# Performance work log

Measured on AMD Instinct MI355X. Metric: run time of the kernel, lower is better.

The kernel has to match this reference:

```python
import jax, jax.numpy as jnp
import numpy as np

B, C, T, H, W = 4, 256, 16, 16, 16
C2 = C // 2  # 128


def setup_inputs() -> dict:
    key = jax.random.key(0)
    ks = jax.random.split(key, 12)
    s = 1.0 / np.sqrt(C)
    return {
        "X": jax.random.normal(ks[0], (B, C, T, H, W), dtype=jnp.float32),
        "pe": jax.random.uniform(ks[1], (C, T, H, W), dtype=jnp.float32),
        "task_q": jax.random.uniform(ks[2], (C2, T, H, W), dtype=jnp.float32),
        "task_k": jax.random.uniform(ks[3], (C2, T, H, W), dtype=jnp.float32),
        "task_v": jax.random.uniform(ks[4], (C2, T, H, W), dtype=jnp.float32),
        "Wq": jax.random.normal(ks[5], (C2, C), dtype=jnp.float32) * s,
        "bq": jnp.zeros((C2,), dtype=jnp.float32),
        "Wk": jax.random.normal(ks[6], (C2, C), dtype=jnp.float32) * s,
        "bk": jnp.zeros((C2,), dtype=jnp.float32),
        "Wv": jax.random.normal(ks[7], (C2, C), dtype=jnp.float32) * s,
        "bv": jnp.zeros((C2,), dtype=jnp.float32),
        "Wo": jax.random.normal(ks[8], (C, C2), dtype=jnp.float32) * s,
    }


def reference(X, pe, task_q, task_k, task_v, Wq, bq, Wk, bk, Wv, bv, Wo):
    b, c, t, h, w = X.shape
    c2 = Wq.shape[0]
    n = t * h * w
    Xp = X + pe  # broadcast [C,T,H,W] over batch

    def proj(Wm, bm, task):
        # 1x1x1 Conv3d == channel contraction; add bias and per-task offset
        y = jnp.einsum('bcthw,oc->bothw', Xp, Wm)
        return y + bm[:, None, None, None] + task  # [B,C2,T,H,W]

    q = proj(Wq, bq, task_q).reshape(b, c2, n).transpose(0, 2, 1)  # [B,N,C2]
    k = proj(Wk, bk, task_k).reshape(b, c2, n)                     # [B,C2,N]
    sim = jnp.matmul(q, k)                                         # [B,N,N]
    v = proj(Wv, bv, task_v).reshape(b, c2, n).transpose(0, 2, 1)  # [B,N,C2]
    # NOTE: original torch code computes softmax(sim) but then multiplies by
    # the RAW similarity matrix (softmax output is dead code). Faithful math:
    out = jnp.matmul(sim, v)                                       # [B,N,C2]
    # torch .reshape of contiguous [B,N,C2] -> [B,C2,T,H,W] (layout reinterpret)
    out = out.reshape(b, c2, t, h, w)
    out = jnp.einsum('bcthw,oc->bothw', out, Wo)  # out_conv, no bias
    return out + X
```

## Files before the change

kernel.cpp:

```cpp
#include <hip/hip_runtime.h>
#include <cstddef>

#define BB 4
#define CCH 256
#define C2 128
#define NN 4096
#define PM 384
#define KVS 16

typedef __attribute__((ext_vector_type(8))) short short8v;
typedef __attribute__((ext_vector_type(4))) short short4v;
typedef __attribute__((ext_vector_type(4))) float f32x4;

static __device__ __forceinline__ short f2bf(float f) {
    union { float f; unsigned u; } c; c.f = f;
    unsigned r = (c.u + 0x7FFFu + ((c.u >> 16) & 1u)) >> 16;
    return (short)r;
}

__global__ __launch_bounds__(256) void k_pack(
    const float* __restrict__ Wq, const float* __restrict__ bq,
    const float* __restrict__ Wk, const float* __restrict__ bk,
    const float* __restrict__ Wv, const float* __restrict__ bv,
    const float* __restrict__ Wo,
    short* __restrict__ wpackh, float* __restrict__ bpack,
    short* __restrict__ Woh)
{
    const int m = blockIdx.x;
    const int c = threadIdx.x;
    if (m < PM) {
        const float* w; const float* bs; int mm;
        if (m < C2)        { w = Wq; bs = bq; mm = m; }
        else if (m < 2*C2) { w = Wk; bs = bk; mm = m - C2; }
        else               { w = Wv; bs = bv; mm = m - 2*C2; }
        wpackh[m * CCH + c] = f2bf(w[mm * CCH + c]);
        if (c == 0) bpack[m] = bs[mm];
    } else {
        const int o = m - PM;
        if (c < C2) Woh[o * C2 + c] = f2bf(Wo[o * C2 + c]);
    }
}

#define LROW 40
#define TSP  136
__global__ __launch_bounds__(256) void k_projm(
    const float* __restrict__ X, const float* __restrict__ pe,
    const float* __restrict__ tq, const float* __restrict__ tk,
    const float* __restrict__ tv,
    const short* __restrict__ wpackh, const float* __restrict__ bpack,
    short* __restrict__ qt, short* __restrict__ kk, short* __restrict__ vv)
{
    __shared__ short smem[17408];
    short* As = smem;
    short* Bs = smem + 5120;
    const int b  = blockIdx.z;
    const int m0 = blockIdx.y * 128;
    const int n0 = blockIdx.x * 128;
    const int tid  = threadIdx.x;
    const int wave = tid >> 6;
    const int lane = tid & 63;
    const int lr = lane & 15, lg = lane >> 4;
    const int wm = wave >> 1, wn = wave & 1;
    const float* __restrict__ Xb = X + (size_t)b * CCH * NN;

    const int am  = tid >> 1;
    const int akb = tid & 1;
    const int cq  = tid >> 5;
    const int nq  = tid & 31;

    f32x4 acc[4][4];
#pragma unroll
    for (int i = 0; i < 4; ++i)
#pragma unroll
        for (int j = 0; j < 4; ++j) acc[i][j] = (f32x4){0.f, 0.f, 0.f, 0.f};

    for (int k0 = 0; k0 < CCH; k0 += 32) {
        {
            const size_t gsrc = (size_t)(m0 + am) * CCH + k0 + akb * 16;
            *(short8v*)&As[am * LROW + akb * 16]     = *(const short8v*)&wpackh[gsrc];
            *(short8v*)&As[am * LROW + akb * 16 + 8] = *(const short8v*)&wpackh[gsrc + 8];
        }
        short sreg[4][4];
#pragma unroll
        for (int j = 0; j < 4; ++j) {
            const int c = k0 + cq * 4 + j;
            const size_t g = (size_t)c * NN + n0 + nq * 4;
            float4 x4 = *(const float4*)&Xb[g];
            float4 p4 = *(const float4*)&pe[g];
            sreg[j][0] = f2bf(x4.x + p4.x);
            sreg[j][1] = f2bf(x4.y + p4.y);
            sreg[j][2] = f2bf(x4.z + p4.z);
            sreg[j][3] = f2bf(x4.w + p4.w);
        }
#pragma unroll
        for (int i = 0; i < 4; ++i) {
            short4v v; v.x = sreg[0][i]; v.y = sreg[1][i]; v.z = sreg[2][i]; v.w = sreg[3][i];
            *(short4v*)&Bs[(nq * 4 + i) * LROW + cq * 4] = v;
        }
        __syncthreads();
        short8v a[4], bfr[4];
#pragma unroll
        for (int fm = 0; fm < 4; ++fm)
            a[fm] = *(const short8v*)&As[(wm * 64 + fm * 16 + lr) * LROW + lg * 8];
#pragma unroll
        for (int fn = 0; fn < 4; ++fn)
            bfr[fn] = *(const short8v*)&Bs[(wn * 64 + fn * 16 + lr) * LROW + lg * 8];
#pragma unroll
        for (int fm = 0; fm < 4; ++fm)
#pragma unroll
            for (int fn = 0; fn < 4; ++fn)
                acc[fm][fn] = __builtin_amdgcn_mfma_f32_16x16x32_bf16(
                    a[fm], bfr[fn], acc[fm][fn], 0, 0, 0);
        __syncthreads();
    }

    short* Ts = smem;
    const int sel = m0 >> 7;
    if (sel == 0) {
#pragma unroll
        for (int fm = 0; fm < 4; ++fm)
#pragma unroll
            for (int fn = 0; fn < 4; ++fn) {
                const int n_l  = wn * 64 + fn * 16 + lr;
                const int m_lb = wm * 64 + fm * 16 + lg * 4;
                short4v v;
#pragma unroll
                for (int r = 0; r < 4; ++r) {
                    const int m_l = m_lb + r;
                    v[r] = f2bf(acc[fm][fn][r] + bpack[m_l]
                                + tq[(size_t)m_l * NN + n0 + n_l]);
                }
                *(short4v*)&Ts[n_l * TSP + m_lb] = v;
            }
        __syncthreads();
        const int n_l = tid >> 1, half = tid & 1;
        short* dst = qt + (size_t)b * NN * C2 + (size_t)(n0 + n_l) * C2 + half * 64;
        const short* src = &Ts[n_l * TSP + half * 64];
#pragma unroll
        for (int q2 = 0; q2 < 8; ++q2)
            *(short8v*)&dst[q2 * 8] = *(const short8v*)&src[q2 * 8];
    } else {
        const float* __restrict__ task = (sel == 1) ? tk : tv;
        short* kv = (sel == 1) ? kk : vv;
#pragma unroll
        for (int fm = 0; fm < 4; ++fm)
#pragma unroll
            for (int fn = 0; fn < 4; ++fn) {
                const int n_l = wn * 64 + fn * 16 + lr;
#pragma unroll
                for (int r = 0; r < 4; ++r) {
                    const int m_l = wm * 64 + fm * 16 + lg * 4 + r;
                    Ts[m_l * TSP + n_l] =
                        f2bf(acc[fm][fn][r] + bpack[m0 + m_l]
                             + task[(size_t)m_l * NN + n0 + n_l]);
                }
            }
        __syncthreads();
        const int m_l = tid >> 1, half = tid & 1;
        short* dst = kv + (size_t)b * C2 * NN + (size_t)m_l * NN + n0 + half * 64;
        const short* src = &Ts[m_l * TSP + half * 64];
#pragma unroll
        for (int q2 = 0; q2 < 8; ++q2)
            *(short8v*)&dst[q2 * 8] = *(const short8v*)&src[q2 * 8];
    }
}

__global__ __launch_bounds__(256) void k_kv(
    const short* __restrict__ kk, const short* __restrict__ vv,
    float* __restrict__ Mpart)
{
    const int b = blockIdx.y, s = blockIdx.x;
    const int tid = threadIdx.x;
    const int wave = tid >> 6, lane = tid & 63;
    const int lr = lane & 15, lg = lane >> 4;
    const int wi = wave >> 1, wj = wave & 1;
    const short* Kb = kk + (size_t)b * C2 * NN;
    const short* Vb = vv + (size_t)b * C2 * NN;
    const int nbase = s * 256;
    f32x4 acc[4][4];
#pragma unroll
    for (int i = 0; i < 4; ++i)
#pragma unroll
        for (int j = 0; j < 4; ++j) acc[i][j] = (f32x4){0.f, 0.f, 0.f, 0.f};

    for (int ks = 0; ks < 8; ++ks) {
        const int nn = nbase + ks * 32 + lg * 8;
        short8v a[4], bv8[4];
#pragma unroll
        for (int fi = 0; fi < 4; ++fi)
            a[fi] = *(const short8v*)&Kb[(size_t)(wi * 64 + fi * 16 + lr) * NN + nn];
#pragma unroll
        for (int fj = 0; fj < 4; ++fj)
            bv8[fj] = *(const short8v*)&Vb[(size_t)(wj * 64 + fj * 16 + lr) * NN + nn];
#pragma unroll
        for (int fi = 0; fi < 4; ++fi)
#pragma unroll
            for (int fj = 0; fj < 4; ++fj)
                acc[fi][fj] = __builtin_amdgcn_mfma_f32_16x16x32_bf16(
                    a[fi], bv8[fj], acc[fi][fj], 0, 0, 0);
    }
    float* Mp = Mpart + ((size_t)b * KVS + s) * C2 * C2;
#pragma unroll
    for (int fi = 0; fi < 4; ++fi)
#pragma unroll
        for (int fj = 0; fj < 4; ++fj) {
            const int j = wj * 64 + fj * 16 + lr;
#pragma unroll
            for (int r = 0; r < 4; ++r) {
                const int i = wi * 64 + fi * 16 + lg * 4 + r;
                Mp[(size_t)i * C2 + j] = acc[fi][fj][r];
            }
        }
}

__global__ __launch_bounds__(256) void k_kvred(
    const float* __restrict__ Mpart, short* __restrict__ Mt)
{
    const int b = blockIdx.y;
    const int i = blockIdx.x * 16 + (threadIdx.x >> 4);
    const int j0 = (threadIdx.x & 15) * 8;
    const float* p = Mpart + (size_t)b * KVS * C2 * C2 + (size_t)i * C2 + j0;
    float a8[8];
#pragma unroll
    for (int e = 0; e < 8; ++e) a8[e] = 0.f;
    for (int s = 0; s < KVS; ++s) {
        float4 v0 = *(const float4*)&p[(size_t)s * C2 * C2];
        float4 v1 = *(const float4*)&p[(size_t)s * C2 * C2 + 4];
        a8[0] += v0.x; a8[1] += v0.y; a8[2] += v0.z; a8[3] += v0.w;
        a8[4] += v1.x; a8[5] += v1.y; a8[6] += v1.z; a8[7] += v1.w;
    }
    short* mt = Mt + (size_t)b * C2 * C2;
#pragma unroll
    for (int e = 0; e < 8; ++e)
        mt[(size_t)(j0 + e) * C2 + i] = f2bf(a8[e]);
}

__global__ __launch_bounds__(256) void k_qm(
    const short* __restrict__ qt, const short* __restrict__ Mt,
    short* __restrict__ out3)
{
    const int b = blockIdx.y;
    const int n0 = blockIdx.x * 128;
    const int tid = threadIdx.x;
    const int wave = tid >> 6, lane = tid & 63;
    const int lr = lane & 15, lg = lane >> 4;
    const int wj = wave >> 1, wn = wave & 1;
    const short* Mb = Mt + (size_t)b * C2 * C2;
    const short* Qb = qt + (size_t)b * NN * C2;
    f32x4 acc[4][4];
#pragma unroll
    for (int i = 0; i < 4; ++i)
#pragma unroll
        for (int j = 0; j < 4; ++j) acc[i][j] = (f32x4){0.f, 0.f, 0.f, 0.f};

    for (int ks = 0; ks < 4; ++ks) {
        const int kb = ks * 32 + lg * 8;
        short8v a[4], bq8[4];
#pragma unroll
        for (int fj = 0; fj < 4; ++fj)
            a[fj] = *(const short8v*)&Mb[(size_t)(wj * 64 + fj * 16 + lr) * C2 + kb];
#pragma unroll
        for (int fn = 0; fn < 4; ++fn)
            bq8[fn] = *(const short8v*)&Qb[(size_t)(n0 + wn * 64 + fn * 16 + lr) * C2 + kb];
#pragma unroll
        for (int fj = 0; fj < 4; ++fj)
#pragma unroll
            for (int fn = 0; fn < 4; ++fn)
                acc[fj][fn] = __builtin_amdgcn_mfma_f32_16x16x32_bf16(
                    a[fj], bq8[fn], acc[fj][fn], 0, 0, 0);
    }
    short* O3 = out3 + (size_t)b * NN * C2;
#pragma unroll
    for (int fj = 0; fj < 4; ++fj)
#pragma unroll
        for (int fn = 0; fn < 4; ++fn) {
            const int n  = n0 + wn * 64 + fn * 16 + lr;
            const int jb = wj * 64 + fj * 16 + lg * 4;
            short4v v;
#pragma unroll
            for (int r = 0; r < 4; ++r) v[r] = f2bf(acc[fj][fn][r]);
            *(short4v*)&O3[(size_t)n * C2 + jb] = v;
        }
}

__global__ __launch_bounds__(256) void k_final(
    const short* __restrict__ out3, const short* __restrict__ Woh,
    const float* __restrict__ X, float* __restrict__ out)
{
    const int g  = blockIdx.x;
    const int o0 = blockIdx.y * 128;
    const int b  = blockIdx.z;
    const int tid = threadIdx.x;
    const int wave = tid >> 6, lane = tid & 63;
    const int lr = lane & 15, lg = lane >> 4;
    const int wm = wave >> 1, wn = wave & 1;
    const short* O3 = out3 + (size_t)b * NN * C2;
    f32x4 acc[4][4];
#pragma unroll
    for (int i = 0; i < 4; ++i)
#pragma unroll
        for (int j = 0; j < 4; ++j) acc[i][j] = (f32x4){0.f, 0.f, 0.f, 0.f};

    for (int ks = 0; ks < 4; ++ks) {
        const int c0 = ks * 32;
        short8v a[4], bb[4];
#pragma unroll
        for (int fm = 0; fm < 4; ++fm)
            a[fm] = *(const short8v*)&Woh[(size_t)(o0 + wm * 64 + fm * 16 + lr) * C2
                                          + c0 + lg * 8];
#pragma unroll
        for (int fn = 0; fn < 4; ++fn) {
            const int pj = wn * 64 + fn * 16 + lr;
            short8v t;
#pragma unroll
            for (int e = 0; e < 8; ++e)
                t[e] = O3[(size_t)((c0 + lg * 8 + e) * 32 + g) * C2 + pj];
            bb[fn] = t;
        }
#pragma unroll
        for (int fm = 0; fm < 4; ++fm)
#pragma unroll
            for (int fn = 0; fn < 4; ++fn)
                acc[fm][fn] = __builtin_amdgcn_mfma_f32_16x16x32_bf16(
                    a[fm], bb[fn], acc[fm][fn], 0, 0, 0);
    }
    const float* Xb = X + (size_t)b * CCH * NN;
    float* Ob = out + (size_t)b * CCH * NN;
#pragma unroll
    for (int fm = 0; fm < 4; ++fm)
#pragma unroll
        for (int fn = 0; fn < 4; ++fn) {
            const int p  = g * 128 + wn * 64 + fn * 16 + lr;
            const int ob = o0 + wm * 64 + fm * 16 + lg * 4;
#pragma unroll
            for (int r = 0; r < 4; ++r) {
                const size_t ad = (size_t)(ob + r) * NN + p;
                Ob[ad] = acc[fm][fn][r] + Xb[ad];
            }
        }
}

extern "C" void kernel_launch(void* const* d_in, const int* in_sizes, int n_in,
                              void* d_out, int out_size, void* d_ws, size_t ws_size,
                              hipStream_t stream) {
    const float* X  = (const float*)d_in[0];
    const float* pe = (const float*)d_in[1];
    const float* tq = (const float*)d_in[2];
    const float* tk = (const float*)d_in[3];
    const float* tv = (const float*)d_in[4];
    const float* Wq = (const float*)d_in[5];
    const float* bq = (const float*)d_in[6];
    const float* Wk = (const float*)d_in[7];
    const float* bk = (const float*)d_in[8];
    const float* Wv = (const float*)d_in[9];
    const float* bv = (const float*)d_in[10];
    const float* Wo = (const float*)d_in[11];
    float* out = (float*)d_out;

    float* ws     = (float*)d_ws;
    float* bpack  = ws;
    short* wpackh = (short*)(ws + 512);
    short* Woh    = (short*)(ws + 512 + 49152);
    short* qt     = (short*)(ws + 512 + 49152 + 16384);
    short* kk     = qt + (size_t)BB * NN * C2;
    short* vv     = kk + (size_t)BB * NN * C2;
    short* out3   = vv + (size_t)BB * NN * C2;
    short* Mt     = out3 + (size_t)BB * NN * C2;
    float* Mpart  = (float*)(Mt + (size_t)BB * C2 * C2);

    k_pack<<<dim3(PM + CCH), dim3(256), 0, stream>>>(
        Wq, bq, Wk, bk, Wv, bv, Wo, wpackh, bpack, Woh);
    k_projm<<<dim3(NN / 128, 3, BB), dim3(256), 0, stream>>>(
        X, pe, tq, tk, tv, wpackh, bpack, qt, kk, vv);
    k_kv<<<dim3(KVS, BB), dim3(256), 0, stream>>>(kk, vv, Mpart);
    k_kvred<<<dim3(8, BB), dim3(256), 0, stream>>>(Mpart, Mt);
    k_qm<<<dim3(NN / 128, BB), dim3(256), 0, stream>>>(qt, Mt, out3);
    k_final<<<dim3(32, 2, BB), dim3(256), 0, stream>>>(out3, Woh, X, out);
}
```

Before: 139.3 us.

## Precompute bf16 X+pe, split KV reduction finer, fuse Q·M with output projection

Adds a pre-pass that converts X+pe to bf16 once, so the projection kernel no longer re-reads and re-adds fp32 X and pe for each of its three row blocks. The K·V partial reduction is split into twice as many slices for more parallelism. The Q·M product and the output 1x1 conv are fused into one kernel that holds the intermediate tile in shared memory instead of writing and re-reading out3. The cost is an extra launch and a workspace buffer for Xp, which Mpart now shares (aliases).

New measurement: 149.1 us. 1.07x slower.

```diff
diff --git a/kernel.cpp b/kernel.cpp
--- a/kernel.cpp
+++ b/kernel.cpp
@@ -6,7 +6,7 @@
 #define C2 128
 #define NN 4096
 #define PM 384
-#define KVS 16
+#define KVS 32
 
 typedef __attribute__((ext_vector_type(8))) short short8v;
 typedef __attribute__((ext_vector_type(4))) short short4v;
@@ -41,10 +41,28 @@
     }
 }
 
+__global__ __launch_bounds__(256) void k_xph(
+    const float* __restrict__ X, const float* __restrict__ pe,
+    short* __restrict__ XpH)
+{
+    const size_t e8 = ((size_t)blockIdx.x * 256 + threadIdx.x) * 8;
+    const size_t r  = e8 & (size_t)(CCH * NN - 1);
+    float4 x0 = *(const float4*)&X[e8];
+    float4 x1 = *(const float4*)&X[e8 + 4];
+    float4 p0 = *(const float4*)&pe[r];
+    float4 p1 = *(const float4*)&pe[r + 4];
+    short8v o;
+    o[0] = f2bf(x0.x + p0.x); o[1] = f2bf(x0.y + p0.y);
+    o[2] = f2bf(x0.z + p0.z); o[3] = f2bf(x0.w + p0.w);
+    o[4] = f2bf(x1.x + p1.x); o[5] = f2bf(x1.y + p1.y);
+    o[6] = f2bf(x1.z + p1.z); o[7] = f2bf(x1.w + p1.w);
+    *(short8v*)&XpH[e8] = o;
+}
+
 #define LROW 40
 #define TSP  136
 __global__ __launch_bounds__(256) void k_projm(
-    const float* __restrict__ X, const float* __restrict__ pe,
+    const short* __restrict__ XpH,
     const float* __restrict__ tq, const float* __restrict__ tk,
     const float* __restrict__ tv,
     const short* __restrict__ wpackh, const float* __restrict__ bpack,
@@ -61,7 +79,7 @@
     const int lane = tid & 63;
     const int lr = lane & 15, lg = lane >> 4;
     const int wm = wave >> 1, wn = wave & 1;
-    const float* __restrict__ Xb = X + (size_t)b * CCH * NN;
+    const short* __restrict__ Xb = XpH + (size_t)b * CCH * NN;
 
     const int am  = tid >> 1;
     const int akb = tid & 1;
@@ -84,13 +102,8 @@
 #pragma unroll
         for (int j = 0; j < 4; ++j) {
             const int c = k0 + cq * 4 + j;
-            const size_t g = (size_t)c * NN + n0 + nq * 4;
-            float4 x4 = *(const float4*)&Xb[g];
-            float4 p4 = *(const float4*)&pe[g];
-            sreg[j][0] = f2bf(x4.x + p4.x);
-            sreg[j][1] = f2bf(x4.y + p4.y);
-            sreg[j][2] = f2bf(x4.z + p4.z);
-            sreg[j][3] = f2bf(x4.w + p4.w);
+            short4v xv = *(const short4v*)&Xb[(size_t)c * NN + n0 + nq * 4];
+            sreg[j][0] = xv.x; sreg[j][1] = xv.y; sreg[j][2] = xv.z; sreg[j][3] = xv.w;
         }
 #pragma unroll
         for (int i = 0; i < 4; ++i) {
@@ -176,14 +189,14 @@
     const int wi = wave >> 1, wj = wave & 1;
     const short* Kb = kk + (size_t)b * C2 * NN;
     const short* Vb = vv + (size_t)b * C2 * NN;
-    const int nbase = s * 256;
+    const int nbase = s * 128;
     f32x4 acc[4][4];
 #pragma unroll
     for (int i = 0; i < 4; ++i)
 #pragma unroll
         for (int j = 0; j < 4; ++j) acc[i][j] = (f32x4){0.f, 0.f, 0.f, 0.f};
 
-    for (int ks = 0; ks < 8; ++ks) {
+    for (int ks = 0; ks < 4; ++ks) {
         const int nn = nbase + ks * 32 + lg * 8;
         short8v a[4], bv8[4];
 #pragma unroll
@@ -235,109 +248,102 @@
         mt[(size_t)(j0 + e) * C2 + i] = f2bf(a8[e]);
 }
 
-__global__ __launch_bounds__(256) void k_qm(
+#define PSP 136
+__global__ __launch_bounds__(256) void k_qmfinal(
     const short* __restrict__ qt, const short* __restrict__ Mt,
-    short* __restrict__ out3)
-{
-    const int b = blockIdx.y;
-    const int n0 = blockIdx.x * 128;
-    const int tid = threadIdx.x;
-    const int wave = tid >> 6, lane = tid & 63;
-    const int lr = lane & 15, lg = lane >> 4;
-    const int wj = wave >> 1, wn = wave & 1;
-    const short* Mb = Mt + (size_t)b * C2 * C2;
-    const short* Qb = qt + (size_t)b * NN * C2;
-    f32x4 acc[4][4];
-#pragma unroll
-    for (int i = 0; i < 4; ++i)
-#pragma unroll
-        for (int j = 0; j < 4; ++j) acc[i][j] = (f32x4){0.f, 0.f, 0.f, 0.f};
-
-    for (int ks = 0; ks < 4; ++ks) {
-        const int kb = ks * 32 + lg * 8;
-        short8v a[4], bq8[4];
-#pragma unroll
-        for (int fj = 0; fj < 4; ++fj)
-            a[fj] = *(const short8v*)&Mb[(size_t)(wj * 64 + fj * 16 + lr) * C2 + kb];
-#pragma unroll
-        for (int fn = 0; fn < 4; ++fn)
-            bq8[fn] = *(const short8v*)&Qb[(size_t)(n0 + wn * 64 + fn * 16 + lr) * C2 + kb];
-#pragma unroll
-        for (int fj = 0; fj < 4; ++fj)
-#pragma unroll
-            for (int fn = 0; fn < 4; ++fn)
-                acc[fj][fn] = __builtin_amdgcn_mfma_f32_16x16x32_bf16(
-                    a[fj], bq8[fn], acc[fj][fn], 0, 0, 0);
-    }
-    short* O3 = out3 + (size_t)b * NN * C2;
-#pragma unroll
-    for (int fj = 0; fj < 4; ++fj)
-#pragma unroll
-        for (int fn = 0; fn < 4; ++fn) {
-            const int n  = n0 + wn * 64 + fn * 16 + lr;
-            const int jb = wj * 64 + fj * 16 + lg * 4;
-            short4v v;
-#pragma unroll
-            for (int r = 0; r < 4; ++r) v[r] = f2bf(acc[fj][fn][r]);
-            *(short4v*)&O3[(size_t)n * C2 + jb] = v;
-        }
-}
-
-__global__ __launch_bounds__(256) void k_final(
-    const short* __restrict__ out3, const short* __restrict__ Woh,
+    const short* __restrict__ Woh,
     const float* __restrict__ X, float* __restrict__ out)
 {
+    __shared__ short Ps[64 * PSP];
     const int g  = blockIdx.x;
-    const int o0 = blockIdx.y * 128;
+    const int jh = blockIdx.y;
     const int b  = blockIdx.z;
     const int tid = threadIdx.x;
     const int wave = tid >> 6, lane = tid & 63;
     const int lr = lane & 15, lg = lane >> 4;
-    const int wm = wave >> 1, wn = wave & 1;
-    const short* O3 = out3 + (size_t)b * NN * C2;
-    f32x4 acc[4][4];
-#pragma unroll
-    for (int i = 0; i < 4; ++i)
-#pragma unroll
-        for (int j = 0; j < 4; ++j) acc[i][j] = (f32x4){0.f, 0.f, 0.f, 0.f};
-
-    for (int ks = 0; ks < 4; ++ks) {
-        const int c0 = ks * 32;
-        short8v a[4], bb[4];
-#pragma unroll
-        for (int fm = 0; fm < 4; ++fm)
-            a[fm] = *(const short8v*)&Woh[(size_t)(o0 + wm * 64 + fm * 16 + lr) * C2
-                                          + c0 + lg * 8];
-#pragma unroll
-        for (int fn = 0; fn < 4; ++fn) {
-            const int pj = wn * 64 + fn * 16 + lr;
-            short8v t;
-#pragma unroll
-            for (int e = 0; e < 8; ++e)
-                t[e] = O3[(size_t)((c0 + lg * 8 + e) * 32 + g) * C2 + pj];
-            bb[fn] = t;
-        }
-#pragma unroll
-        for (int fm = 0; fm < 4; ++fm)
-#pragma unroll
-            for (int fn = 0; fn < 4; ++fn)
-                acc[fm][fn] = __builtin_amdgcn_mfma_f32_16x16x32_bf16(
-                    a[fm], bb[fn], acc[fm][fn], 0, 0, 0);
-    }
-    const float* Xb = X + (size_t)b * CCH * NN;
-    float* Ob = out + (size_t)b * CCH * NN;
-#pragma unroll
-    for (int fm = 0; fm < 4; ++fm)
-#pragma unroll
-        for (int fn = 0; fn < 4; ++fn) {
-            const int p  = g * 128 + wn * 64 + fn * 16 + lr;
-            const int ob = o0 + wm * 64 + fm * 16 + lg * 4;
-#pragma unroll
-            for (int r = 0; r < 4; ++r) {
-                const size_t ad = (size_t)(ob + r) * NN + p;
-                Ob[ad] = acc[fm][fn][r] + Xb[ad];
-            }
-        }
+    const short* Qb = qt + (size_t)b * NN * C2;
+    const short* Mb = Mt + (size_t)b * C2 * C2;
+
+    {
+        const int wc = wave >> 1, wj = wave & 1;
+        f32x4 acc1[4][2];
+#pragma unroll
+        for (int i = 0; i < 4; ++i)
+#pragma unroll
+            for (int j = 0; j < 2; ++j) acc1[i][j] = (f32x4){0.f, 0.f, 0.f, 0.f};
+        for (int ks = 0; ks < 4; ++ks) {
+            const int kb = ks * 32 + lg * 8;
+            short8v a1[4], b1[2];
+#pragma unroll
+            for (int fc = 0; fc < 4; ++fc) {
+                const int c = wc * 64 + fc * 16 + lr;
+                a1[fc] = *(const short8v*)&Qb[(size_t)(c * 32 + g) * C2 + kb];
+            }
+#pragma unroll
+            for (int fj = 0; fj < 2; ++fj) {
+                const int j = jh * 64 + wj * 32 + fj * 16 + lr;
+                b1[fj] = *(const short8v*)&Mb[(size_t)j * C2 + kb];
+            }
+#pragma unroll
+            for (int fc = 0; fc < 4; ++fc)
+#pragma unroll
+                for (int fj = 0; fj < 2; ++fj)
+                    acc1[fc][fj] = __builtin_amdgcn_mfma_f32_16x16x32_bf16(
+                        a1[fc], b1[fj], acc1[fc][fj], 0, 0, 0);
+        }
+#pragma unroll
+        for (int fc = 0; fc < 4; ++fc)
+#pragma unroll
+            for (int fj = 0; fj < 2; ++fj) {
+                const int jp = wj * 32 + fj * 16 + lr;
+                const int c0 = wc * 64 + fc * 16 + lg * 4;
+                short4v v;
+#pragma unroll
+                for (int r = 0; r < 4; ++r) v[r] = f2bf(acc1[fc][fj][r]);
+                *(short4v*)&Ps[jp * PSP + c0] = v;
+            }
+    }
+    __syncthreads();
+
+    {
+        f32x4 acc2[4][4];
+#pragma unroll
+        for (int i = 0; i < 4; ++i)
+#pragma unroll
+            for (int j = 0; j < 4; ++j) acc2[i][j] = (f32x4){0.f, 0.f, 0.f, 0.f};
+        for (int ks = 0; ks < 4; ++ks) {
+            const int kb = ks * 32 + lg * 8;
+            short8v a2[4], b2[4];
+#pragma unroll
+            for (int fo = 0; fo < 4; ++fo) {
+                const int o = wave * 64 + fo * 16 + lr;
+                a2[fo] = *(const short8v*)&Woh[(size_t)o * C2 + kb];
+            }
+#pragma unroll
+            for (int fj = 0; fj < 4; ++fj)
+                b2[fj] = *(const short8v*)&Ps[(fj * 16 + lr) * PSP + kb];
+#pragma unroll
+            for (int fo = 0; fo < 4; ++fo)
+#pragma unroll
+                for (int fj = 0; fj < 4; ++fj)
+                    acc2[fo][fj] = __builtin_amdgcn_mfma_f32_16x16x32_bf16(
+                        a2[fo], b2[fj], acc2[fo][fj], 0, 0, 0);
+        }
+        const float* Xb = X + (size_t)b * CCH * NN;
+        float* Ob = out + (size_t)b * CCH * NN;
+#pragma unroll
+        for (int fo = 0; fo < 4; ++fo)
+#pragma unroll
+            for (int fj = 0; fj < 4; ++fj) {
+                const int p = g * 128 + jh * 64 + fj * 16 + lr;
+                const int ob = wave * 64 + fo * 16 + lg * 4;
+#pragma unroll
+                for (int r = 0; r < 4; ++r) {
+                    const size_t ad = (size_t)(ob + r) * NN + p;
+                    Ob[ad] = acc2[fo][fj][r] + Xb[ad];
+                }
+            }
+    }
 }
 
 extern "C" void kernel_launch(void* const* d_in, const int* in_sizes, int n_in,
@@ -364,16 +370,16 @@
     short* qt     = (short*)(ws + 512 + 49152 + 16384);
     short* kk     = qt + (size_t)BB * NN * C2;
     short* vv     = kk + (size_t)BB * NN * C2;
-    short* out3   = vv + (size_t)BB * NN * C2;
-    short* Mt     = out3 + (size_t)BB * NN * C2;
-    float* Mpart  = (float*)(Mt + (size_t)BB * C2 * C2);
+    short* Mt     = vv + (size_t)BB * NN * C2;
+    short* XpH    = Mt + (size_t)BB * C2 * C2;
+    float* Mpart  = (float*)XpH;
 
     k_pack<<<dim3(PM + CCH), dim3(256), 0, stream>>>(
         Wq, bq, Wk, bk, Wv, bv, Wo, wpackh, bpack, Woh);
+    k_xph<<<dim3((BB * CCH * NN) / (256 * 8)), dim3(256), 0, stream>>>(X, pe, XpH);
     k_projm<<<dim3(NN / 128, 3, BB), dim3(256), 0, stream>>>(
-        X, pe, tq, tk, tv, wpackh, bpack, qt, kk, vv);
+        XpH, tq, tk, tv, wpackh, bpack, qt, kk, vv);
     k_kv<<<dim3(KVS, BB), dim3(256), 0, stream>>>(kk, vv, Mpart);
     k_kvred<<<dim3(8, BB), dim3(256), 0, stream>>>(Mpart, Mt);
-    k_qm<<<dim3(NN / 128, BB), dim3(256), 0, stream>>>(qt, Mt, out3);
-    k_final<<<dim3(32, 2, BB), dim3(256), 0, stream>>>(out3, Woh, X, out);
-}
+    k_qmfinal<<<dim3(32, 2, BB), dim3(256), 0, stream>>>(qt, Mt, Woh, X, out);
+}
```
